# Kernel tuning notes

Measured on AMD Instinct MI355X. Metric: run time of the kernel, lower is better.

## Reference

```python
import jax, jax.numpy as jnp
import numpy as np
from jax import lax

A_RATIOS = (0.5, 1.0, 2.0)
A_SCALES = (8, 16, 32)
FEAT_STRIDE = 16
BASE_SIZE = 16
PRE_NMS = 6000     # n_test_pre_nms
POST_NMS = 300     # n_test_post_nms
NMS_THRESH = 0.7
MIN_SIZE = 16.0
SCALE = 1.0        # forward(scale=1.0) default
NEG = -1e10


def _anchor_base():
    # standard generate_anchor_base: centered at (8,8), ratios x scales
    py = px = BASE_SIZE / 2.0
    rows = []
    for r in A_RATIOS:
        for s in A_SCALES:
            h = BASE_SIZE * s * np.sqrt(r)
            w = BASE_SIZE * s * np.sqrt(1.0 / r)
            rows.append([py - h / 2.0, px - w / 2.0, py + h / 2.0, px + w / 2.0])
    return np.asarray(rows, np.float32)  # (A, 4)


def _all_anchors(height, width):
    base = jnp.asarray(_anchor_base())                                  # (A, 4)
    sy = (jnp.arange(height) * FEAT_STRIDE).astype(jnp.float32)
    sx = (jnp.arange(width) * FEAT_STRIDE).astype(jnp.float32)
    gy, gx = jnp.meshgrid(sy, sx, indexing='ij')
    shift = jnp.stack([gy.ravel(), gx.ravel(), gy.ravel(), gx.ravel()], axis=1)  # (K, 4)
    anch = base[None, :, :] + shift[:, None, :]                         # (K, A, 4)
    return anch.reshape(-1, 4)                                          # (K*A, 4)


def _conv(x, w, b, pad):
    y = lax.conv_general_dilated(x, w, (1, 1), [(pad, pad), (pad, pad)],
                                 dimension_numbers=('NCHW', 'OIHW', 'NCHW'))
    return y + b[None, :, None, None]


def _loc2bbox(anchors, locs):
    h = anchors[:, 2] - anchors[:, 0]
    w = anchors[:, 3] - anchors[:, 1]
    cy = anchors[:, 0] + 0.5 * h
    cx = anchors[:, 1] + 0.5 * w
    dy, dx, dh, dw = locs[:, 0], locs[:, 1], locs[:, 2], locs[:, 3]
    ncy = dy * h + cy
    ncx = dx * w + cx
    nh = jnp.exp(dh) * h
    nw = jnp.exp(dw) * w
    return jnp.stack([ncy - 0.5 * nh, ncx - 0.5 * nw,
                      ncy + 0.5 * nh, ncx + 0.5 * nw], axis=1)


def _iou_one_vs_all(box, boxes):
    ty = jnp.maximum(box[0], boxes[:, 0])
    tx = jnp.maximum(box[1], boxes[:, 1])
    by = jnp.minimum(box[2], boxes[:, 2])
    bx = jnp.minimum(box[3], boxes[:, 3])
    inter = jnp.maximum(by - ty, 0.0) * jnp.maximum(bx - tx, 0.0)
    a1 = (box[2] - box[0]) * (box[3] - box[1])
    a2 = (boxes[:, 2] - boxes[:, 0]) * (boxes[:, 3] - boxes[:, 1])
    return inter / (a1 + a2 - inter + 1e-9)


def _nms(boxes, scores):
    # greedy NMS with fixed POST_NMS output; invalid slots are zero boxes
    def step(s, _):
        i = jnp.argmax(s)
        valid = s[i] > NEG / 2
        ious = _iou_one_vs_all(boxes[i], boxes)
        s = jnp.where(ious > NMS_THRESH, NEG, s)  # suppresses self (iou=1)
        return s, (i, valid)
    _, (idx, valid) = lax.scan(step, scores, None, length=POST_NMS)
    return boxes[idx] * valid[:, None].astype(boxes.dtype)  # (POST_NMS, 4)


def _proposals(anchors, locs, fg, img_h, img_w):
    boxes = _loc2bbox(anchors, locs)
    boxes = jnp.stack([jnp.clip(boxes[:, 0], 0.0, img_h),
                       jnp.clip(boxes[:, 1], 0.0, img_w),
                       jnp.clip(boxes[:, 2], 0.0, img_h),
                       jnp.clip(boxes[:, 3], 0.0, img_w)], axis=1)
    hs = boxes[:, 2] - boxes[:, 0]
    ws = boxes[:, 3] - boxes[:, 1]
    ok = (hs >= MIN_SIZE * SCALE) & (ws >= MIN_SIZE * SCALE)
    sc = jnp.where(ok, fg, NEG)
    top_sc, idx = lax.top_k(sc, PRE_NMS)
    return _nms(boxes[idx], top_sc)


def reference(base_feat, W_conv1, b_conv1, W_score, b_score, W_loc, b_loc, img_h, img_w):
    N, _, H, W = base_feat.shape
    A = 9
    mid = jax.nn.relu(_conv(base_feat, W_conv1, b_conv1, 1))            # (N,512,H,W)
    rpn_locs = _conv(mid, W_loc, b_loc, 0).transpose(0, 2, 3, 1).reshape(N, H * W * A, 4)
    raw = _conv(mid, W_score, b_score, 0).transpose(0, 2, 3, 1)          # (N,H,W,2A)
    rpn_scores = raw.reshape(N, H * W * A, 2)
    fg = jax.nn.softmax(raw.reshape(N, H, W, A, 2), axis=-1)[..., 1].reshape(N, -1)
    anchors = _all_anchors(H, W)                                         # (H*W*A,4)
    ih, iw = float(img_h), float(img_w)
    prop = jax.vmap(lambda l, f: _proposals(anchors, l, f, ih, iw))(rpn_locs, fg)
    rois = prop.reshape(N * POST_NMS, 4)
    roi_indices = jnp.repeat(jnp.arange(N, dtype=jnp.int32), POST_NMS)
    return rpn_locs, rpn_scores, rois, roi_indices, anchors


def setup_inputs() -> dict:
    key = jax.random.key(0)
    k0, k1, k2, k3 = jax.random.split(key, 4)
    N, C, H, W = 4, 512, 64, 64
    nA = 9
    return {
        'base_feat': jax.random.normal(k0, (N, C, H, W), jnp.float32),
        'W_conv1': 0.01 * jax.random.normal(k1, (512, 512, 3, 3), jnp.float32),
        'b_conv1': jnp.zeros((512,), jnp.float32),
        'W_score': 0.01 * jax.random.normal(k2, (2 * nA, 512, 1, 1), jnp.float32),
        'b_score': jnp.zeros((2 * nA,), jnp.float32),
        'W_loc': 0.01 * jax.random.normal(k3, (4 * nA, 512, 1, 1), jnp.float32),
        'b_loc': jnp.zeros((4 * nA,), jnp.float32),
        'img_h': 1024,
        'img_w': 1024,
    }
```

## Files before the change

### kernel.cpp

```cpp
#include <hip/hip_runtime.h>
#include <math.h>

#define HH 64
#define WW 64
#define NIMG 4
#define CIN 512
#define AA 9
#define HWA (HH*WW*AA)
#define PRE_NMS 6000
#define POST_NMS 300
#define NEGV (-1e10f)
#define NEGK 0xD01502F9u
#define NWORD 94

#define OFF1 589824
#define OFF2 884736
#define OFF3 889536
#define OFF4 890736

typedef unsigned int u32;
typedef unsigned long long u64;
typedef _Float16 f16;
typedef _Float16 half8 __attribute__((ext_vector_type(8)));
typedef float f32x4 __attribute__((ext_vector_type(4)));

__device__ __forceinline__ void gload_lds16(const void* g, void* l)
{
    __builtin_amdgcn_global_load_lds((const __attribute__((address_space(1))) void*)g,
                                     (__attribute__((address_space(3))) void*)l,
                                     16, 0, 0);
}

__global__ __launch_bounds__(256) void k_prep_x(const float* __restrict__ x,
                                                f16* __restrict__ xh,
                                                f16* __restrict__ xl)
{
    __shared__ float tile[64][65];
    int ci0 = blockIdx.x * 64, y = blockIdx.y, n = blockIdx.z;
    int t = threadIdx.x;
    #pragma unroll
    for (int l = 0; l < 16; ++l) {
        int idx = l * 256 + t;
        int cc = idx >> 6, xc = idx & 63;
        tile[cc][xc] = x[((size_t)(n * CIN + ci0 + cc) * HH + y) * WW + xc];
    }
    __syncthreads();
    #pragma unroll
    for (int l = 0; l < 16; ++l) {
        int idx = l * 256 + t;
        int xc = idx >> 6, cc = idx & 63;
        float v = tile[cc][xc];
        f16 hi = (f16)v;
        f16 lo = (f16)(v - (float)hi);
        size_t o = ((size_t)(n * 64 + y) * 64 + xc) * 512 + ci0 + cc;
        xh[o] = hi; xl[o] = lo;
    }
}

__global__ __launch_bounds__(256) void k_prep_w(const float* __restrict__ W1,
                                                f16* __restrict__ wh,
                                                f16* __restrict__ wl)
{
    int idx = blockIdx.x * 256 + threadIdx.x;
    int co = idx >> 9, ci = idx & 511;
    #pragma unroll
    for (int tap = 0; tap < 9; ++tap) {
        float v = W1[(size_t)idx * 9 + tap];
        f16 hi = (f16)v;
        f16 lo = (f16)(v - (float)hi);
        size_t o = ((size_t)tap * 512 + co) * 512 + ci;
        wh[o] = hi; wl[o] = lo;
    }
}

__global__ __launch_bounds__(256, 4) void k_conv_mfma(const f16* __restrict__ xh,
                                                      const f16* __restrict__ xl,
                                                      const f16* __restrict__ wh,
                                                      const f16* __restrict__ wl,
                                                      const float* __restrict__ bias,
                                                      float* __restrict__ mid)
{
    __shared__ f16 sX[2][4][64][32];
    const int t = threadIdx.x;
    const int yb = blockIdx.x, co0 = blockIdx.y * 64, n = blockIdx.z;
    const int y0 = yb * 2;
    const int wv = t >> 6, lane = t & 63;
    const int q = lane >> 4, li = lane & 15;
    const int mh = wv & 1;
    const int xhp = wv >> 1;

    if (yb == 0 || yb == 31) {
        int rowu = (yb == 0) ? 0 : 3072;
        u32* p = (u32*)&sX[0][0][0][0];
        #pragma unroll
        for (int l = 0; l < 8; ++l) {
            int idx = l * 256 + t;
            int plane = idx >> 10, r = idx & 1023;
            p[plane * 4096 + rowu + r] = 0;
        }
    }

    f32x4 acc[2][2][2];
    #pragma unroll
    for (int mt = 0; mt < 2; ++mt)
        #pragma unroll
        for (int xn = 0; xn < 2; ++xn)
            #pragma unroll
            for (int yy = 0; yy < 2; ++yy)
                acc[mt][xn][yy] = (f32x4){0.f, 0.f, 0.f, 0.f};

    auto prefetch = [&](int ci0) {
        #pragma unroll
        for (int m = 0; m < 8; ++m) {
            int k2 = wv * 8 + m;
            int plane = k2 >> 4;
            int row = (k2 >> 2) & 3;
            int gy = y0 - 1 + row;
            if ((unsigned)gy < 64u) {
                int col = ((k2 & 3) << 4) + (lane >> 2);
                int s = lane & 3;
                const f16* src = (plane ? xl : xh) +
                    (((size_t)(n * 64 + gy) * 64 + col) * 512 + ci0 + s * 8);
                f16* dst = &sX[0][0][0][0] + (size_t)k2 * 512 + lane * 8;
                gload_lds16(src, dst);
            }
        }
    };

    half8 wa[2][2], wn[2][2];
    auto loadW = [&](half8 w[2][2], int ci0, int tap) {
        #pragma unroll
        for (int mt = 0; mt < 2; ++mt) {
            size_t base = ((size_t)(tap * 512) + co0 + mh * 32 + mt * 16 + li) * 512 + ci0 + q * 8;
            w[0][mt] = *(const half8*)(wh + base);
            w[1][mt] = *(const half8*)(wl + base);
        }
    };

    prefetch(0);
    loadW(wa, 0, 0);

    const half8 zero8 = {(f16)0, (f16)0, (f16)0, (f16)0, (f16)0, (f16)0, (f16)0, (f16)0};

    for (int chunk = 0; chunk < 16; ++chunk) {
        const int ci0 = chunk * 32;
        __syncthreads();

        #pragma unroll
        for (int tap = 0; tap < 9; ++tap) {
            if (tap < 8) loadW(wn, ci0, tap + 1);
            const int ky = tap / 3, kx = tap - ky * 3;

            half8 B[2][2][2];
            #pragma unroll
            for (int xn = 0; xn < 2; ++xn) {
                int xc = xhp * 32 + xn * 16 + li;
                int colr = xc + kx - 1;
                bool oob = (colr < 0) || (colr > 63);
                int colc = oob ? 0 : colr;
                #pragma unroll
                for (int yy = 0; yy < 2; ++yy) {
                    int row = yy + ky;
                    const f16* ph = &sX[0][row][colc][q * 8];
                    half8 vh = *(const half8*)ph;
                    half8 vl = *(const half8*)(ph + 8192);
                    if (oob) { vh = zero8; vl = zero8; }
                    B[0][xn][yy] = vh; B[1][xn][yy] = vl;
                }
            }
            #pragma unroll
            for (int mt = 0; mt < 2; ++mt)
                #pragma unroll
                for (int xn = 0; xn < 2; ++xn)
                    #pragma unroll
                    for (int yy = 0; yy < 2; ++yy)
                        acc[mt][xn][yy] = __builtin_amdgcn_mfma_f32_16x16x32_f16(wa[0][mt], B[0][xn][yy], acc[mt][xn][yy], 0, 0, 0);
            #pragma unroll
            for (int mt = 0; mt < 2; ++mt)
                #pragma unroll
                for (int xn = 0; xn < 2; ++xn)
                    #pragma unroll
                    for (int yy = 0; yy < 2; ++yy)
                        acc[mt][xn][yy] = __builtin_amdgcn_mfma_f32_16x16x32_f16(wa[0][mt], B[1][xn][yy], acc[mt][xn][yy], 0, 0, 0);
            #pragma unroll
            for (int mt = 0; mt < 2; ++mt)
                #pragma unroll
                for (int xn = 0; xn < 2; ++xn)
                    #pragma unroll
                    for (int yy = 0; yy < 2; ++yy)
                        acc[mt][xn][yy] = __builtin_amdgcn_mfma_f32_16x16x32_f16(wa[1][mt], B[0][xn][yy], acc[mt][xn][yy], 0, 0, 0);

            if (tap < 8) {
                #pragma unroll
                for (int pl = 0; pl < 2; ++pl)
                    #pragma unroll
                    for (int mt = 0; mt < 2; ++mt) wa[pl][mt] = wn[pl][mt];
            }
        }

        if (chunk + 1 < 16) {
            __syncthreads();
            prefetch(ci0 + 32);
            loadW(wa, ci0 + 32, 0);
        }
    }

    #pragma unroll
    for (int mt = 0; mt < 2; ++mt) {
        #pragma unroll
        for (int r = 0; r < 4; ++r) {
            int co = co0 + mh * 32 + mt * 16 + q * 4 + r;
            float bv = bias[co];
            #pragma unroll
            for (int xn = 0; xn < 2; ++xn) {
                int xc = xhp * 32 + xn * 16 + li;
                #pragma unroll
                for (int yy = 0; yy < 2; ++yy) {
                    float v = acc[mt][xn][yy][r] + bv;
                    mid[((size_t)(n * 512 + co) * HH + y0 + yy) * WW + xc] = v > 0.f ? v : 0.f;
                }
            }
        }
    }
}

__global__ __launch_bounds__(256) void k_htrans(const float* __restrict__ Ws,
                                                const float* __restrict__ Wl,
                                                float* __restrict__ Wt2)
{
    int i = blockIdx.x * 256 + threadIdx.x;
    if (i >= 512 * 64) return;
    int ci = i >> 6, co = i & 63;
    float v = 0.f;
    if (co < 18) v = Ws[co * 512 + ci];
    else if (co < 54) v = Wl[(co - 18) * 512 + ci];
    Wt2[i] = v;
}

__global__ __launch_bounds__(256) void k_hgemm(const float* __restrict__ mid,
                                               const float* __restrict__ Wt2,
                                               float* __restrict__ sraw)
{
    __shared__ float sM[32][64];
    __shared__ float sW2[32][64];
    const int t = threadIdx.x;
    const int px0 = blockIdx.x * 64, n = blockIdx.y;
    const int tx = t & 15, ty = t >> 4;

    float acc[4][4];
    #pragma unroll
    for (int c = 0; c < 4; ++c)
        #pragma unroll
        for (int j = 0; j < 4; ++j) acc[c][j] = 0.f;

    for (int ci0 = 0; ci0 < 512; ci0 += 32) {
        __syncthreads();
        #pragma unroll
        for (int l = 0; l < 8; ++l) {
            int i = l * 256 + t;
            int ci = i >> 6, px = i & 63;
            sM[ci][px] = mid[((size_t)n * 512 + ci0 + ci) * 4096 + px0 + px];
            sW2[ci][px] = Wt2[(size_t)(ci0 + ci) * 64 + px];
        }
        __syncthreads();
        #pragma unroll
        for (int ci = 0; ci < 32; ++ci) {
            float mv[4], wv[4];
            #pragma unroll
            for (int j = 0; j < 4; ++j) mv[j] = sM[ci][tx * 4 + j];
            #pragma unroll
            for (int c = 0; c < 4; ++c) wv[c] = sW2[ci][ty * 4 + c];
            #pragma unroll
            for (int c = 0; c < 4; ++c)
                #pragma unroll
                for (int j = 0; j < 4; ++j) acc[c][j] += wv[c] * mv[j];
        }
    }
    #pragma unroll
    for (int c = 0; c < 4; ++c) {
        float4 v = make_float4(acc[c][0], acc[c][1], acc[c][2], acc[c][3]);
        *(float4*)&sraw[((size_t)n * 64 + ty * 4 + c) * 4096 + px0 + tx * 4] = v;
    }
}

__global__ __launch_bounds__(256) void k_decode(const float* __restrict__ sraw,
                                                const float* __restrict__ bsc,
                                                const float* __restrict__ blc,
                                                const int* __restrict__ ph,
                                                const int* __restrict__ pw,
                                                float* __restrict__ out,
                                                float* __restrict__ boxes,
                                                u32* __restrict__ key)
{
    int p = blockIdx.x * 256 + threadIdx.x;
    int n = p >> 12, pi = p & 4095;
    int y = pi >> 6, xq = pi & 63;

    const float* S = sraw + (size_t)n * 64 * 4096 + pi;
    float* o0 = out + (size_t)n * 147456;
    float* o1 = out + OFF1 + (size_t)n * 73728;
    float IHf = (float)(*ph), IWf = (float)(*pw);

    #pragma unroll
    for (int a = 0; a < 9; ++a) {
        float s0 = S[(size_t)(2 * a) * 4096] + bsc[2 * a];
        float s1 = S[(size_t)(2 * a + 1) * 4096] + bsc[2 * a + 1];
        float dy = S[(size_t)(18 + 4 * a) * 4096] + blc[4 * a];
        float dx = S[(size_t)(19 + 4 * a) * 4096] + blc[4 * a + 1];
        float dh = S[(size_t)(20 + 4 * a) * 4096] + blc[4 * a + 2];
        float dw = S[(size_t)(21 + 4 * a) * 4096] + blc[4 * a + 3];

        o1[(pi * 9 + a) * 2 + 0] = s0;
        o1[(pi * 9 + a) * 2 + 1] = s1;
        o0[(pi * 9 + a) * 4 + 0] = dy;
        o0[(pi * 9 + a) * 4 + 1] = dx;
        o0[(pi * 9 + a) * 4 + 2] = dh;
        o0[(pi * 9 + a) * 4 + 3] = dw;

        float mm = fmaxf(s0, s1);
        float e0 = expf(s0 - mm), e1 = expf(s1 - mm);
        float fg = e1 / (e0 + e1);

        int ri = a / 3, si = a - ri * 3;
        double s = (double)(8 << si);
        double rr = (ri == 0) ? 0.5 : ((ri == 1) ? 1.0 : 2.0);
        double hh = 16.0 * s * sqrt(rr);
        double wd = 16.0 * s * sqrt(1.0 / rr);
        float a0 = (float)(8.0 - hh * 0.5) + (float)(y * 16);
        float a1 = (float)(8.0 - wd * 0.5) + (float)(xq * 16);
        float a2 = (float)(8.0 + hh * 0.5) + (float)(y * 16);
        float a3 = (float)(8.0 + wd * 0.5) + (float)(xq * 16);

        float h = a2 - a0, w = a3 - a1;
        float cy = a0 + 0.5f * h, cx = a1 + 0.5f * w;
        float ncy = dy * h + cy, ncx = dx * w + cx;
        float nh = expf(dh) * h, nw = expf(dw) * w;
        float b0 = fminf(fmaxf(ncy - 0.5f * nh, 0.f), IHf);
        float b1 = fminf(fmaxf(ncx - 0.5f * nw, 0.f), IWf);
        float b2 = fminf(fmaxf(ncy + 0.5f * nh, 0.f), IHf);
        float b3 = fminf(fmaxf(ncx + 0.5f * nw, 0.f), IWf);

        bool ok = (b2 - b0 >= 16.0f) && (b3 - b1 >= 16.0f);
        float sc = ok ? fg : NEGV;

        int gi = n * HWA + pi * 9 + a;
        ((float4*)boxes)[gi] = make_float4(b0, b1, b2, b3);
        u32 u = __float_as_uint(sc);
        u32 kasc = (u & 0x80000000u) ? ~u : (u | 0x80000000u);
        key[gi] = ~kasc;
    }
}

__global__ void k_misc(float* __restrict__ out)
{
    int i = blockIdx.x * 256 + threadIdx.x;
    if (i < 4800) out[OFF2 + i] = 0.f;
    if (i < 1200) out[OFF3 + i] = (float)(i / 300);
    if (i < HWA) {
        int pi = i / 9, a = i - pi * 9;
        int y = pi >> 6, xq = pi & 63;
        int ri = a / 3, si = a - ri * 3;
        double s = (double)(8 << si);
        double rr = (ri == 0) ? 0.5 : ((ri == 1) ? 1.0 : 2.0);
        double hh = 16.0 * s * sqrt(rr);
        double wd = 16.0 * s * sqrt(1.0 / rr);
        out[OFF4 + i * 4 + 0] = (float)(8.0 - hh * 0.5) + (float)(y * 16);
        out[OFF4 + i * 4 + 1] = (float)(8.0 - wd * 0.5) + (float)(xq * 16);
        out[OFF4 + i * 4 + 2] = (float)(8.0 + hh * 0.5) + (float)(y * 16);
        out[OFF4 + i * 4 + 3] = (float)(8.0 + wd * 0.5) + (float)(xq * 16);
    }
}

__global__ __launch_bounds__(1024) void k_select(const u32* __restrict__ key,
                                                 u64* __restrict__ cmp,
                                                 int* __restrict__ nvalid)
{
    __shared__ int hist[256];
    __shared__ u32 sPref;
    __shared__ int sR;
    __shared__ int cLess, cEq, cVal;
    int n = blockIdx.x, t = threadIdx.x;
    const u32* k0 = key + (size_t)n * HWA;

    u32 pref = 0, mask = 0;
    int R = PRE_NMS;
    for (int pass = 0; pass < 4; ++pass) {
        int shift = 24 - pass * 8;
        if (t < 256) hist[t] = 0;
        __syncthreads();
        for (int i = t; i < HWA; i += 1024) {
            u32 k = k0[i];
            if ((k & mask) == pref) atomicAdd(&hist[(k >> shift) & 255], 1);
        }
        __syncthreads();
        if (t == 0) {
            int cum = 0;
            for (int b = 0; b < 256; ++b) {
                int c = hist[b];
                if (cum + c >= R) { sPref = pref | ((u32)b << shift); sR = R - cum; break; }
                cum += c;
            }
        }
        __syncthreads();
        pref = sPref; R = sR; mask |= (0xFFu << shift);
        __syncthreads();
    }
    u32 T = pref;
    if (t == 0) { cLess = 0; cEq = 0; cVal = 0; }
    __syncthreads();
    for (int i = t; i < HWA; i += 1024) {
        u32 k = k0[i];
        if (k < NEGK) atomicAdd(&cVal, 1);
        if (k < T) {
            int p = atomicAdd(&cLess, 1);
            cmp[(size_t)n * 8192 + p] = ((u64)k << 32) | (u32)i;
        } else if (k == T) {
            int p = atomicAdd(&cEq, 1);
            if (p < R) cmp[(size_t)n * 8192 + (PRE_NMS - 1 - p)] = ((u64)k << 32) | (u32)i;
        }
    }
    __syncthreads();
    if (t == 0) nvalid[n] = cVal < PRE_NMS ? cVal : PRE_NMS;
}

__global__ __launch_bounds__(256) void k_rank2(const u64* __restrict__ cmp,
                                               const float* __restrict__ boxes,
                                               float* __restrict__ boxesS)
{
    __shared__ u64 sK[PRE_NMS];
    int n = blockIdx.y;
    int t = threadIdx.x;
    const u64* K = cmp + (size_t)n * 8192;
    for (int j = t; j < PRE_NMS; j += 256) sK[j] = K[j];
    __syncthreads();
    int i = blockIdx.x * 256 + t;
    if (i >= PRE_NMS) return;
    u64 ki = sK[i];
    int rank = 0;
    #pragma unroll 8
    for (int j = 0; j < PRE_NMS; ++j)
        rank += (sK[j] < ki) ? 1 : 0;
    u32 idx = (u32)(ki & 0xFFFFFFFFu);
    ((float4*)boxesS)[(size_t)n * PRE_NMS + rank] =
        ((const float4*)boxes)[(size_t)n * HWA + idx];
}

__global__ __launch_bounds__(64) void k_iou(const float* __restrict__ boxesS,
                                            u64* __restrict__ mask)
{
    __shared__ float4 cb[64];
    int w = blockIdx.x, ic = blockIdx.y, n = blockIdx.z;
    if (w < ic) return;
    int t = threadIdx.x;
    const float4* B = (const float4*)boxesS + (size_t)n * PRE_NMS;
    int jc = w * 64 + t;
    cb[t] = (jc < PRE_NMS) ? B[jc] : make_float4(0.f, 0.f, 0.f, 0.f);
    __syncthreads();
    int i = ic * 64 + t;
    if (i >= PRE_NMS) return;
    float4 bb = B[i];
    float area1 = (bb.z - bb.x) * (bb.w - bb.y);
    u64 m = 0;
    #pragma unroll 8
    for (int j = 0; j < 64; ++j) {
        float4 o = cb[j];
        float ty_ = fmaxf(bb.x, o.x), tx_ = fmaxf(bb.y, o.y);
        float by_ = fminf(bb.z, o.z), bx_ = fminf(bb.w, o.w);
        float inter = fmaxf(by_ - ty_, 0.f) * fmaxf(bx_ - tx_, 0.f);
        float area2 = (o.z - o.x) * (o.w - o.y);
        float iou = inter / (area1 + area2 - inter + 1e-9f);
        if (iou > 0.7f) m |= (1ull << j);
    }
    mask[((size_t)n * PRE_NMS + i) * NWORD + w] = m;
}

__global__ __launch_bounds__(64) void k_nms4(const u64* __restrict__ mask,
                                             const int* __restrict__ nvalid,
                                             const float* __restrict__ boxesS,
                                             float* __restrict__ rois)
{
    int n = blockIdx.x, lane = threadIdx.x;
    int nv = nvalid[n];
    const u64* M = mask + (size_t)n * PRE_NMS * NWORD;
    const float4* B = (const float4*)boxesS + (size_t)n * PRE_NMS;

    auto vmask = [&](int w) -> u64 {
        int lo = w * 64;
        if (nv >= lo + 64) return ~0ull;
        if (nv <= lo) return 0ull;
        return (1ull << (nv - lo)) - 1ull;
    };
    u64 vm0 = vmask(lane);
    u64 vm1 = (lane < NWORD - 64) ? vmask(64 + lane) : 0ull;
    u64 rem0 = 0, rem1 = 0;

    int cnt = 0;
    while (cnt < POST_NMS) {
        u64 t0 = (~rem0) & vm0;
        u64 t1 = (~rem1) & vm1;
        int cand[8];
        int nc = 0;
        #pragma unroll
        for (int k = 0; k < 8; ++k) {
            u64 b0 = __ballot(t0 != 0);
            int c = -1;
            if (b0) {
                int l = __builtin_ctzll(b0);
                u64 w = __shfl(t0, l);
                c = l * 64 + __builtin_ctzll(w);
                if (lane == l) t0 &= t0 - 1;
            } else {
                u64 b1 = __ballot(t1 != 0);
                if (b1) {
                    int l = __builtin_ctzll(b1);
                    u64 w = __shfl(t1, l);
                    c = (64 + l) * 64 + __builtin_ctzll(w);
                    if (lane == l) t1 &= t1 - 1;
                }
            }
            if (c < 0) break;
            cand[nc++] = c;
        }
        if (nc == 0) break;

        u64 r0[8], r1[8];
        for (int k = 0; k < nc; ++k) {
            const u64* Mr = M + (size_t)cand[k] * NWORD;
            r0[k] = Mr[lane];
            r1[k] = (lane < NWORD - 64) ? Mr[64 + lane] : 0ull;
        }

        for (int k = 0; k < nc && cnt < POST_NMS; ++k) {
            int c = cand[k];
            int w = c >> 6, b = c & 63;
            u64 cw = (w < 64) ? __shfl(rem0, w) : __shfl(rem1, w - 64);
            if (!((cw >> b) & 1ull)) {
                if (lane == 0) {
                    float4 bb = B[c];
                    float* orow = rois + (size_t)(n * POST_NMS + cnt) * 4;
                    orow[0] = bb.x; orow[1] = bb.y; orow[2] = bb.z; orow[3] = bb.w;
                }
                rem0 |= r0[k];
                rem1 |= r1[k];
                cnt++;
            }
        }
    }
}

extern "C" void kernel_launch(void* const* d_in, const int* in_sizes, int n_in,
                              void* d_out, int out_size, void* d_ws, size_t ws_size,
                              hipStream_t stream)
{
    const float* x  = (const float*)d_in[0];
    const float* W1 = (const float*)d_in[1];
    const float* b1 = (const float*)d_in[2];
    const float* Ws = (const float*)d_in[3];
    const float* bs = (const float*)d_in[4];
    const float* Wl = (const float*)d_in[5];
    const float* bl = (const float*)d_in[6];
    const int* ih   = (const int*)d_in[7];
    const int* iw   = (const int*)d_in[8];
    float* out = (float*)d_out;
    char* ws = (char*)d_ws;

    f16*   Wh2    = (f16*)  (ws);
    f16*   Wl2    = (f16*)  (ws + 4718592);
    float* mid    = (float*)(ws + 9437184);
    f16*   xh     = (f16*)  (ws + 42991616);
    f16*   xl     = (f16*)  (ws + 59768832);
    float* boxes  = (float*)(ws + 42991616);
    u32*   key    = (u32*)  (ws + 45350912);
    u64*   cmp    = (u64*)  (ws + 45940736);
    float* boxesS = (float*)(ws + 46202880);
    int*   nval   = (int*)  (ws + 46586880);
    float* Wt2    = (float*)(ws);
    float* sraw   = (float*)(ws + 262144);
    u64*   iomask = (u64*)  (ws + 9437184);

    k_prep_x<<<dim3(8, 64, 4), 256, 0, stream>>>(x, xh, xl);
    k_prep_w<<<1024, 256, 0, stream>>>(W1, Wh2, Wl2);
    k_conv_mfma<<<dim3(32, 8, 4), 256, 0, stream>>>(xh, xl, Wh2, Wl2, b1, mid);
    k_htrans<<<128, 256, 0, stream>>>(Ws, Wl, Wt2);
    k_hgemm<<<dim3(64, 4), 256, 0, stream>>>(mid, Wt2, sraw);
    k_decode<<<64, 256, 0, stream>>>(sraw, bs, bl, ih, iw, out, boxes, key);
    k_misc<<<144, 256, 0, stream>>>(out);
    k_select<<<4, 1024, 0, stream>>>(key, cmp, nval);
    k_rank2<<<dim3(24, NIMG), 256, 0, stream>>>(cmp, boxes, boxesS);
    k_iou<<<dim3(NWORD, NWORD, NIMG), 64, 0, stream>>>(boxesS, iomask);
    k_nms4<<<NIMG, 64, 0, stream>>>(iomask, nval, boxesS, out + OFF2);
}
```

Before: 915.7 us.

## Split hi/lo input planes into separate LDS buffers to overlap loads with MFMA

After: 992.4 us. +8.4%, slower.

```diff
diff --git a/kernel.cpp b/kernel.cpp
--- a/kernel.cpp
+++ b/kernel.cpp
@@ -73,14 +73,15 @@
     }
 }
 
-__global__ __launch_bounds__(256, 4) void k_conv_mfma(const f16* __restrict__ xh,
-                                                      const f16* __restrict__ xl,
+__global__ __launch_bounds__(256, 4) void k_conv_mfma(const f16* __restrict__ xh_,
+                                                      const f16* __restrict__ xl_,
                                                       const f16* __restrict__ wh,
                                                       const f16* __restrict__ wl,
                                                       const float* __restrict__ bias,
                                                       float* __restrict__ mid)
 {
-    __shared__ f16 sX[2][4][64][32];
+    __shared__ f16 sH[4][64][32];
+    __shared__ f16 sL[4][64][32];
     const int t = threadIdx.x;
     const int yb = blockIdx.x, co0 = blockIdx.y * 64, n = blockIdx.z;
     const int y0 = yb * 2;
@@ -91,12 +92,13 @@
 
     if (yb == 0 || yb == 31) {
         int rowu = (yb == 0) ? 0 : 3072;
-        u32* p = (u32*)&sX[0][0][0][0];
-        #pragma unroll
-        for (int l = 0; l < 8; ++l) {
+        u32* pH = (u32*)&sH[0][0][0];
+        u32* pL = (u32*)&sL[0][0][0];
+        #pragma unroll
+        for (int l = 0; l < 4; ++l) {
             int idx = l * 256 + t;
-            int plane = idx >> 10, r = idx & 1023;
-            p[plane * 4096 + rowu + r] = 0;
+            pH[rowu + idx] = 0;
+            pL[rowu + idx] = 0;
         }
     }
 
@@ -109,26 +111,24 @@
             for (int yy = 0; yy < 2; ++yy)
                 acc[mt][xn][yy] = (f32x4){0.f, 0.f, 0.f, 0.f};
 
-    auto prefetch = [&](int ci0) {
-        #pragma unroll
-        for (int m = 0; m < 8; ++m) {
-            int k2 = wv * 8 + m;
-            int plane = k2 >> 4;
-            int row = (k2 >> 2) & 3;
+    auto pf = [&](const f16* srcb, f16* dstb, int ci0) {
+        #pragma unroll
+        for (int m = 0; m < 4; ++m) {
+            int k2 = wv * 4 + m;
+            int row = k2 >> 2;
             int gy = y0 - 1 + row;
             if ((unsigned)gy < 64u) {
                 int col = ((k2 & 3) << 4) + (lane >> 2);
                 int s = lane & 3;
-                const f16* src = (plane ? xl : xh) +
-                    (((size_t)(n * 64 + gy) * 64 + col) * 512 + ci0 + s * 8);
-                f16* dst = &sX[0][0][0][0] + (size_t)k2 * 512 + lane * 8;
-                gload_lds16(src, dst);
+                const f16* src = srcb + (((size_t)(n * 64 + gy) * 64 + col) * 512 + ci0 + s * 8);
+                gload_lds16(src, dstb + (size_t)k2 * 512 + lane * 8);
             }
         }
     };
 
     half8 wa[2][2], wn[2][2];
-    auto loadW = [&](half8 w[2][2], int ci0, int tap) {
+    half8 wb[2], wbn[2];
+    auto loadW2 = [&](half8 w[2][2], int ci0, int tap) {
         #pragma unroll
         for (int mt = 0; mt < 2; ++mt) {
             size_t base = ((size_t)(tap * 512) + co0 + mh * 32 + mt * 16 + li) * 512 + ci0 + q * 8;
@@ -136,22 +136,30 @@
             w[1][mt] = *(const half8*)(wl + base);
         }
     };
-
-    prefetch(0);
-    loadW(wa, 0, 0);
+    auto loadW1 = [&](half8 w[2], int ci0, int tap) {
+        #pragma unroll
+        for (int mt = 0; mt < 2; ++mt) {
+            size_t base = ((size_t)(tap * 512) + co0 + mh * 32 + mt * 16 + li) * 512 + ci0 + q * 8;
+            w[mt] = *(const half8*)(wh + base);
+        }
+    };
 
     const half8 zero8 = {(f16)0, (f16)0, (f16)0, (f16)0, (f16)0, (f16)0, (f16)0, (f16)0};
+
+    pf(xh_, &sH[0][0][0], 0);
 
     for (int chunk = 0; chunk < 16; ++chunk) {
         const int ci0 = chunk * 32;
-        __syncthreads();
+
+        __syncthreads();
+        pf(xl_, &sL[0][0][0], ci0);
+        loadW2(wa, ci0, 0);
 
         #pragma unroll
         for (int tap = 0; tap < 9; ++tap) {
-            if (tap < 8) loadW(wn, ci0, tap + 1);
+            if (tap < 8) loadW2(wn, ci0, tap + 1);
             const int ky = tap / 3, kx = tap - ky * 3;
-
-            half8 B[2][2][2];
+            half8 Bh[2][2];
             #pragma unroll
             for (int xn = 0; xn < 2; ++xn) {
                 int xc = xhp * 32 + xn * 16 + li;
@@ -160,12 +168,8 @@
                 int colc = oob ? 0 : colr;
                 #pragma unroll
                 for (int yy = 0; yy < 2; ++yy) {
-                    int row = yy + ky;
-                    const f16* ph = &sX[0][row][colc][q * 8];
-                    half8 vh = *(const half8*)ph;
-                    half8 vl = *(const half8*)(ph + 8192);
-                    if (oob) { vh = zero8; vl = zero8; }
-                    B[0][xn][yy] = vh; B[1][xn][yy] = vl;
+                    half8 v = *(const half8*)&sH[yy + ky][colc][q * 8];
+                    Bh[xn][yy] = oob ? zero8 : v;
                 }
             }
             #pragma unroll
@@ -174,34 +178,54 @@
                 for (int xn = 0; xn < 2; ++xn)
                     #pragma unroll
                     for (int yy = 0; yy < 2; ++yy)
-                        acc[mt][xn][yy] = __builtin_amdgcn_mfma_f32_16x16x32_f16(wa[0][mt], B[0][xn][yy], acc[mt][xn][yy], 0, 0, 0);
+                        acc[mt][xn][yy] = __builtin_amdgcn_mfma_f32_16x16x32_f16(wa[0][mt], Bh[xn][yy], acc[mt][xn][yy], 0, 0, 0);
             #pragma unroll
             for (int mt = 0; mt < 2; ++mt)
                 #pragma unroll
                 for (int xn = 0; xn < 2; ++xn)
                     #pragma unroll
                     for (int yy = 0; yy < 2; ++yy)
-                        acc[mt][xn][yy] = __builtin_amdgcn_mfma_f32_16x16x32_f16(wa[0][mt], B[1][xn][yy], acc[mt][xn][yy], 0, 0, 0);
+                        acc[mt][xn][yy] = __builtin_amdgcn_mfma_f32_16x16x32_f16(wa[1][mt], Bh[xn][yy], acc[mt][xn][yy], 0, 0, 0);
+            if (tap < 8) {
+                #pragma unroll
+                for (int pl = 0; pl < 2; ++pl)
+                    #pragma unroll
+                    for (int mt = 0; mt < 2; ++mt) wa[pl][mt] = wn[pl][mt];
+            }
+        }
+
+        __syncthreads();
+        if (chunk + 1 < 16) pf(xh_, &sH[0][0][0], ci0 + 32);
+        loadW1(wb, ci0, 0);
+
+        #pragma unroll
+        for (int tap = 0; tap < 9; ++tap) {
+            if (tap < 8) loadW1(wbn, ci0, tap + 1);
+            const int ky = tap / 3, kx = tap - ky * 3;
+            half8 Bl[2][2];
+            #pragma unroll
+            for (int xn = 0; xn < 2; ++xn) {
+                int xc = xhp * 32 + xn * 16 + li;
+                int colr = xc + kx - 1;
+                bool oob = (colr < 0) || (colr > 63);
+                int colc = oob ? 0 : colr;
+                #pragma unroll
+                for (int yy = 0; yy < 2; ++yy) {
+                    half8 v = *(const half8*)&sL[yy + ky][colc][q * 8];
+                    Bl[xn][yy] = oob ? zero8 : v;
+                }
+            }
             #pragma unroll
             for (int mt = 0; mt < 2; ++mt)
                 #pragma unroll
                 for (int xn = 0; xn < 2; ++xn)
                     #pragma unroll
                     for (int yy = 0; yy < 2; ++yy)
-                        acc[mt][xn][yy] = __builtin_amdgcn_mfma_f32_16x16x32_f16(wa[1][mt], B[0][xn][yy], acc[mt][xn][yy], 0, 0, 0);
-
+                        acc[mt][xn][yy] = __builtin_amdgcn_mfma_f32_16x16x32_f16(wb[mt], Bl[xn][yy], acc[mt][xn][yy], 0, 0, 0);
             if (tap < 8) {
                 #pragma unroll
-                for (int pl = 0; pl < 2; ++pl)
-                    #pragma unroll
-                    for (int mt = 0; mt < 2; ++mt) wa[pl][mt] = wn[pl][mt];
-            }
-        }
-
-        if (chunk + 1 < 16) {
-            __syncthreads();
-            prefetch(ci0 + 32);
-            loadW(wa, ci0 + 32, 0);
+                for (int mt = 0; mt < 2; ++mt) wb[mt] = wbn[mt];
+            }
         }
     }
 
```
